# Kernel optimization log

Hardware: AMD Instinct MI355X
Metric: run time of the kernel (lower is better)

The kernel has to match this reference:

```python
import jax, jax.numpy as jnp
import numpy as np

T = 2048        # tokens
HID = 4096      # hidden_size
H = 32          # num attention heads
KV = 8          # num key/value heads (GQA)
D = HID // H    # head_dim = 128
THETA = 10000.0


def setup_inputs() -> dict:
    key = jax.random.key(0)
    k1, k2, k3 = jax.random.split(key, 3)
    hidden_states = jax.random.normal(k1, (T, HID), jnp.float32)
    positions = jnp.arange(T, dtype=jnp.int32)
    Wqkv = jax.random.normal(k2, ((H + 2 * KV) * D, HID), jnp.float32) * 0.02
    Wo = jax.random.normal(k3, (HID, H * D), jnp.float32) * 0.02
    return {"hidden_states": hidden_states, "positions": positions,
            "Wqkv": Wqkv, "Wo": Wo}


def _rope(positions, x):
    """Neox-style rotary embedding. x: [T, h, D], positions: [T]."""
    half = D // 2
    inv_freq = 1.0 / (THETA ** (jnp.arange(half, dtype=jnp.float32) / half))
    ang = positions.astype(jnp.float32)[:, None] * inv_freq      # [T, half]
    cos = jnp.cos(ang)[:, None, :]                                # [T, 1, half]
    sin = jnp.sin(ang)[:, None, :]
    x1, x2 = x[..., :half], x[..., half:]
    return jnp.concatenate([x1 * cos - x2 * sin, x2 * cos + x1 * sin], axis=-1)


def reference(hidden_states, positions, Wqkv, Wo):
    # fused QKV projection (no bias)
    qkv = hidden_states @ Wqkv.T                                  # [T, (H+2KV)*D]
    q, k, v = jnp.split(qkv, [H * D, H * D + KV * D], axis=1)
    q = q.reshape(T, H, D)
    k = k.reshape(T, KV, D)
    v = v.reshape(T, KV, D)
    # RoPE on q and k
    q = _rope(positions, q)
    k = _rope(positions, k)
    # GQA: expand kv heads to match q heads
    g = H // KV
    k = jnp.repeat(k, g, axis=1)                                  # [T, H, D]
    v = jnp.repeat(v, g, axis=1)
    # causal attention (flash-attention math)
    scores = jnp.einsum('thd,shd->hts', q, k) * (D ** -0.5)       # [H, T, T]
    causal = jnp.tril(jnp.ones((T, T), dtype=bool))
    scores = jnp.where(causal[None], scores, jnp.float32(-1e30))
    probs = jax.nn.softmax(scores, axis=-1)
    attn = jnp.einsum('hts,shd->thd', probs, v).reshape(T, H * D)
    # output projection
    return attn @ Wo.T
```

## Files before the change

kernel.cpp:

```cpp
#include <hip/hip_runtime.h>
#include <stdint.h>

#define T_SEQ 2048
#define HIDDEN 4096
#define NHEAD 32
#define NKV 8
#define HDIM 128
#define QKVN 6144

typedef __bf16 bf16x8 __attribute__((ext_vector_type(8)));
typedef float f32x4 __attribute__((ext_vector_type(4)));
typedef unsigned short u16;
typedef u16 u16x8 __attribute__((ext_vector_type(8)));
typedef u16 u16x4 __attribute__((ext_vector_type(4)));

__device__ __forceinline__ u16 f2bf(float f) {
  uint32_t u = __builtin_bit_cast(uint32_t, f);
  u = (u + 0x7fffu + ((u >> 16) & 1u)) >> 16;
  return (u16)u;
}
__device__ __forceinline__ float bf2f(u16 h) {
  uint32_t u = ((uint32_t)h) << 16;
  return __builtin_bit_cast(float, u);
}

__device__ __forceinline__ void gload16(const void* g, void* l) {
  __builtin_amdgcn_global_load_lds(
      (__attribute__((address_space(1))) void*)(uintptr_t)g,
      (__attribute__((address_space(3))) void*)(uintptr_t)l, 16, 0, 0);
}

__global__ void cvt2_kernel(const float* __restrict__ in1, u16* __restrict__ out1, int n1_4,
                            const float* __restrict__ in2, u16* __restrict__ out2, int n2_4) {
  int base = blockIdx.x * blockDim.x + threadIdx.x;
  int stride = gridDim.x * blockDim.x;
  for (int i = base; i < n1_4; i += stride) {
    float4 v = ((const float4*)in1)[i];
    u16x4 o;
    o.x = f2bf(v.x); o.y = f2bf(v.y); o.z = f2bf(v.z); o.w = f2bf(v.w);
    ((u16x4*)out1)[i] = o;
  }
  for (int i = base; i < n2_4; i += stride) {
    float4 v = ((const float4*)in2)[i];
    u16x4 o;
    o.x = f2bf(v.x); o.y = f2bf(v.y); o.z = f2bf(v.z); o.w = f2bf(v.w);
    ((u16x4*)out2)[i] = o;
  }
}

__global__ void prep_kernel(u16* __restrict__ qkv, const int* __restrict__ pos,
                            u16* __restrict__ vt,
                            const float* __restrict__ wo_in, u16* __restrict__ wo_out,
                            int wo_n4) {
  __shared__ u16 tile[64][64];
  const int bid = blockIdx.x;
  const int tid = threadIdx.x;

  if (bid < 512) {
    const int tb = bid & 31;
    const int yy = bid >> 5;
    const int kvh = yy >> 1;
    const int d0 = (yy & 1) * 64;
    const u16* src = qkv + (size_t)(NHEAD + NKV) * HDIM + kvh * HDIM + d0;
#pragma unroll
    for (int g = 0; g < 2; ++g) {
      int u = g * 256 + tid;
      int t = u >> 3, ds = u & 7;
      u16x8 v = *(const u16x8*)(src + (size_t)(tb * 64 + t) * QKVN + ds * 8);
#pragma unroll
      for (int j = 0; j < 8; ++j) {
        int d = ds * 8 + j;
        tile[d][(((t >> 3) ^ (d & 7)) * 8) + (t & 7)] = v[j];
      }
    }
    __syncthreads();
    u16* dst = vt + ((size_t)kvh * HDIM + d0) * T_SEQ + tb * 64;
#pragma unroll
    for (int g = 0; g < 4; ++g) {
      int u = g * 256 + tid;
      int d = u >> 4, qd = u & 15;
      int a = qd >> 3, gg = (qd >> 1) & 3, b = qd & 1;
      int t0 = 32 * a + 16 * b + 4 * gg;
      u16x4 v = *(const u16x4*)&tile[d][(((t0 >> 3) ^ (d & 7)) * 8) + (t0 & 7)];
      *(u16x4*)(dst + (size_t)d * T_SEQ + qd * 4) = v;
    }
    return;
  }

  const int nb = gridDim.x - 512;
  const int base = (bid - 512) * blockDim.x + tid;
  const int stride = nb * blockDim.x;
  for (int idx = base; idx < T_SEQ * 40 * 64; idx += stride) {
    int i = idx & 63;
    int head = (idx >> 6) % 40;
    int t = idx / (40 * 64);
    int hb = head < NHEAD ? head * HDIM : NHEAD * HDIM + (head - NHEAD) * HDIM;
    float p = (float)pos[t];
    float inv_freq = exp2f(-(float)i * (13.287712379549449f / 64.0f));
    float ang = p * inv_freq;
    float s, c;
    sincosf(ang, &s, &c);
    u16* p1 = qkv + (size_t)t * QKVN + hb + i;
    u16* p2 = p1 + 64;
    float x1 = bf2f(*p1), x2 = bf2f(*p2);
    *p1 = f2bf(x1 * c - x2 * s);
    *p2 = f2bf(x2 * c + x1 * s);
  }
  for (int i = base; i < wo_n4; i += stride) {
    float4 v = ((const float4*)wo_in)[i];
    u16x4 o;
    o.x = f2bf(v.x); o.y = f2bf(v.y); o.z = f2bf(v.z); o.w = f2bf(v.w);
    ((u16x4*)wo_out)[i] = o;
  }
}

__device__ __forceinline__ void storeC(float* p, float v) { *p = v; }
__device__ __forceinline__ void storeC(u16* p, float v) { *p = f2bf(v); }
__device__ __forceinline__ f32x4 mfma16(bf16x8 a, bf16x8 b, f32x4 c) {
  return __builtin_amdgcn_mfma_f32_16x16x32_bf16(a, b, c, 0, 0, 0);
}

__global__ void __launch_bounds__(512, 1)
gemm_qkv(const u16* __restrict__ A, const u16* __restrict__ B,
         u16* __restrict__ C, int M, int N, int K) {
  __shared__ u16 As_[2][128 * 64];
  __shared__ u16 Bs_[2][384 * 64];

  const int tid = threadIdx.x;
  const int lane = tid & 63;
  const int w = tid >> 6;
  const int wr = w >> 2, wc = w & 3;
  const int l15 = lane & 15, lg = lane >> 4;

  const int c8 = blockIdx.x & 7, i8 = blockIdx.x >> 3;
  const int by = i8 & 15;
  const int bx = c8 * 2 + (i8 >> 4);
  const int bm = by * 128, bn = bx * 384;

  const int u_lo = w * 64 + lane, u_hi = u_lo + 512;
  const int r0 = u_lo >> 3, s0 = (u_lo & 7) ^ (r0 & 7);
  const int r1 = u_hi >> 3, s1 = (u_hi & 7) ^ (r1 & 7);
  const u16* a_s0 = A + (size_t)(bm + r0) * K + s0 * 8;
  const u16* a_s1 = A + (size_t)(bm + r1) * K + s1 * 8;
  const u16* b_s0[3];
  const u16* b_s1[3];
#pragma unroll
  for (int h = 0; h < 3; ++h) {
    b_s0[h] = B + (size_t)(bn + h * 128 + r0) * K + s0 * 8;
    b_s1[h] = B + (size_t)(bn + h * 128 + r1) * K + s1 * 8;
  }

  const int ax = l15 & 7;
  const int sl0 = (lg ^ ax) * 8;
  const int sl1 = ((4 + lg) ^ ax) * 8;
  const int a_row = (wr * 64 + l15) * 64;
  const int b_row = (wc * 96 + l15) * 64;

  f32x4 acc[4][6] = {};
  bf16x8 af[4][2], bfr[6][2];

#define BARRIER() asm volatile("s_barrier" ::: "memory")
#define WAITBAR(n_) asm volatile("s_waitcnt vmcnt(" #n_ ")\n\ts_barrier" ::: "memory")
#define STAGE_A(t_, p_)                                                        \
  {                                                                            \
    gload16(a_s0 + (size_t)(t_) * 64, &As_[p_][w * 512]);                      \
    gload16(a_s1 + (size_t)(t_) * 64, &As_[p_][4096 + w * 512]);               \
  }
#define STAGE_B(t_, p_, h_)                                                    \
  {                                                                            \
    gload16(b_s0[h_] + (size_t)(t_) * 64, &Bs_[p_][(h_) * 8192 + w * 512]);    \
    gload16(b_s1[h_] + (size_t)(t_) * 64,                                      \
            &Bs_[p_][(h_) * 8192 + 4096 + w * 512]);                           \
  }

  STAGE_A(0, 0);
  STAGE_B(0, 0, 0); STAGE_B(0, 0, 1); STAGE_B(0, 0, 2);
  STAGE_B(1, 1, 0); STAGE_B(1, 1, 1); STAGE_B(1, 1, 2);
  WAITBAR(6);

  const int NT = K >> 6;
  for (int v = 0; v < NT; ++v) {
    const int cur = v & 1, alt = cur ^ 1;
    const u16* Ac = &As_[cur][0];
    const u16* Bc = &Bs_[cur][0];
    const bool s1ok = (v + 1) < NT, s2ok = (v + 2) < NT;

    {
      if (s1ok) STAGE_A(v + 1, alt);
#pragma unroll
      for (int mi = 0; mi < 2; ++mi) {
        af[mi][0] = *(const bf16x8*)&Ac[a_row + mi * 1024 + sl0];
        af[mi][1] = *(const bf16x8*)&Ac[a_row + mi * 1024 + sl1];
      }
#pragma unroll
      for (int ni = 0; ni < 3; ++ni) {
        bfr[ni][0] = *(const bf16x8*)&Bc[b_row + ni * 1024 + sl0];
        bfr[ni][1] = *(const bf16x8*)&Bc[b_row + ni * 1024 + sl1];
      }
      BARRIER();
      __builtin_amdgcn_s_setprio(1);
#pragma unroll
      for (int mi = 0; mi < 2; ++mi)
#pragma unroll
        for (int ni = 0; ni < 3; ++ni) {
          acc[mi][ni] = mfma16(af[mi][0], bfr[ni][0], acc[mi][ni]);
          acc[mi][ni] = mfma16(af[mi][1], bfr[ni][1], acc[mi][ni]);
        }
      __builtin_amdgcn_s_setprio(0);
      BARRIER();
    }
    {
#pragma unroll
      for (int ni = 3; ni < 6; ++ni) {
        bfr[ni][0] = *(const bf16x8*)&Bc[b_row + ni * 1024 + sl0];
        bfr[ni][1] = *(const bf16x8*)&Bc[b_row + ni * 1024 + sl1];
      }
      BARRIER();
      __builtin_amdgcn_s_setprio(1);
#pragma unroll
      for (int mi = 0; mi < 2; ++mi)
#pragma unroll
        for (int ni = 3; ni < 6; ++ni) {
          acc[mi][ni] = mfma16(af[mi][0], bfr[ni][0], acc[mi][ni]);
          acc[mi][ni] = mfma16(af[mi][1], bfr[ni][1], acc[mi][ni]);
        }
      __builtin_amdgcn_s_setprio(0);
      BARRIER();
    }
    {
      if (s2ok) { STAGE_B(v + 2, cur, 0); STAGE_B(v + 2, cur, 1); STAGE_B(v + 2, cur, 2); }
#pragma unroll
      for (int mi = 2; mi < 4; ++mi) {
        af[mi][0] = *(const bf16x8*)&Ac[a_row + mi * 1024 + sl0];
        af[mi][1] = *(const bf16x8*)&Ac[a_row + mi * 1024 + sl1];
      }
      BARRIER();
      __builtin_amdgcn_s_setprio(1);
#pragma unroll
      for (int mi = 2; mi < 4; ++mi)
#pragma unroll
        for (int ni = 0; ni < 6; ++ni) {
          acc[mi][ni] = mfma16(af[mi][0], bfr[ni][0], acc[mi][ni]);
          acc[mi][ni] = mfma16(af[mi][1], bfr[ni][1], acc[mi][ni]);
        }
      __builtin_amdgcn_s_setprio(0);
      if (s2ok) { WAITBAR(6); } else if (s1ok) { WAITBAR(0); } else { BARRIER(); }
    }
  }

#pragma unroll
  for (int mi = 0; mi < 4; ++mi)
#pragma unroll
    for (int ni = 0; ni < 6; ++ni)
#pragma unroll
      for (int r = 0; r < 4; ++r) {
        int row = bm + wr * 64 + mi * 16 + lg * 4 + r;
        int col = bn + wc * 96 + ni * 16 + l15;
        storeC(&C[(size_t)row * N + col], acc[mi][ni][r]);
      }
#undef STAGE_A
#undef STAGE_B
#undef WAITBAR
#undef BARRIER
}

template <typename OutT>
__global__ void __launch_bounds__(512, 2)
gemm256(const u16* __restrict__ A, const u16* __restrict__ B,
        OutT* __restrict__ C0, OutT* __restrict__ C1,
        int N, int K, int NT, int sliceBlocks,
        int nbx, int rw, int rh) {
  __shared__ u16 As_[2][256 * 64];
  __shared__ u16 Bs_[2][256 * 64];

  const int tid = threadIdx.x;
  const int lane = tid & 63;
  const int w = tid >> 6;
  const int wr = w >> 2, wc = w & 3;
  const int l15 = lane & 15, lg = lane >> 4;

  const int bid = blockIdx.x;
  const int slice = bid / sliceBlocks;
  const int wi = bid % sliceBlocks;
  const int k0 = slice * (NT << 6);
  OutT* __restrict__ C = slice ? C1 : C0;

  const int c8 = wi & 7, i8 = wi >> 3;
  const int rpr = nbx / rw;
  const int by = (c8 / rpr) * rh + (i8 % rh);
  const int bx = (c8 % rpr) * rw + (i8 / rh);
  const int bm = by * 256, bn = bx * 256;

  const int u_lo = w * 64 + lane, u_hi = u_lo + 512;
  const int r0 = u_lo >> 3, s0 = (u_lo & 7) ^ (r0 & 7);
  const int r1 = u_hi >> 3, s1 = (u_hi & 7) ^ (r1 & 7);
  const u16* a0s0 = A + (size_t)(bm + r0) * K + k0 + s0 * 8;
  const u16* a0s1 = A + (size_t)(bm + r1) * K + k0 + s1 * 8;
  const u16* a1s0 = A + (size_t)(bm + 128 + r0) * K + k0 + s0 * 8;
  const u16* a1s1 = A + (size_t)(bm + 128 + r1) * K + k0 + s1 * 8;
  const u16* b0s0 = B + (size_t)(bn + r0) * K + k0 + s0 * 8;
  const u16* b0s1 = B + (size_t)(bn + r1) * K + k0 + s1 * 8;
  const u16* b1s0 = B + (size_t)(bn + 128 + r0) * K + k0 + s0 * 8;
  const u16* b1s1 = B + (size_t)(bn + 128 + r1) * K + k0 + s1 * 8;

  const int ax = l15 & 7;
  const int sl0 = (lg ^ ax) * 8;
  const int sl1 = ((4 + lg) ^ ax) * 8;
  const int a_row = (wr * 128 + l15) * 64;
  const int b_row = (wc * 64 + l15) * 64;

  f32x4 acc[8][4] = {};
  bf16x8 bfr[4][2];

#define BARRIER() asm volatile("s_barrier" ::: "memory")
#define WAITBAR(n_) asm volatile("s_waitcnt vmcnt(" #n_ ")\n\ts_barrier" ::: "memory")
#define STAGE_HALF(p0_, p1_, dst_, t_)                                         \
  {                                                                            \
    gload16((p0_) + (size_t)(t_) * 64, (dst_) + (size_t)w * 512);              \
    gload16((p1_) + (size_t)(t_) * 64, (dst_) + 4096 + (size_t)w * 512);       \
  }

  STAGE_HALF(a0s0, a0s1, &As_[0][0], 0);
  STAGE_HALF(a1s0, a1s1, &As_[0][8192], 0);
  STAGE_HALF(b0s0, b0s1, &Bs_[0][0], 0);
  STAGE_HALF(b1s0, b1s1, &Bs_[0][8192], 0);
  STAGE_HALF(b0s0, b0s1, &Bs_[1][0], 1);
  STAGE_HALF(b1s0, b1s1, &Bs_[1][8192], 1);
  WAITBAR(4);

  for (int v = 0; v < NT; ++v) {
    const int cur = v & 1, alt = cur ^ 1;
    const u16* Ac = &As_[cur][0];
    const u16* Bc = &Bs_[cur][0];
    const bool s1ok = (v + 1) < NT, s2ok = (v + 2) < NT;

#define MFMA_QUAD(p_, A0_, A1_, A2_, A3_)                                      \
    __builtin_amdgcn_s_setprio(1);                                             \
    _Pragma("unroll") for (int ni = 0; ni < 4; ++ni) {                         \
      acc[2 * (p_)][ni] = mfma16(A0_, bfr[ni][0], acc[2 * (p_)][ni]);          \
      acc[2 * (p_)][ni] = mfma16(A1_, bfr[ni][1], acc[2 * (p_)][ni]);          \
      acc[2 * (p_) + 1][ni] = mfma16(A2_, bfr[ni][0], acc[2 * (p_) + 1][ni]);  \
      acc[2 * (p_) + 1][ni] = mfma16(A3_, bfr[ni][1], acc[2 * (p_) + 1][ni]);  \
    }                                                                          \
    __builtin_amdgcn_s_setprio(0);

    {
#pragma unroll
      for (int ni = 0; ni < 4; ++ni) {
        bfr[ni][0] = *(const bf16x8*)&Bc[b_row + ni * 1024 + sl0];
        bfr[ni][1] = *(const bf16x8*)&Bc[b_row + ni * 1024 + sl1];
      }
      bf16x8 f0 = *(const bf16x8*)&Ac[a_row + 0 * 1024 + sl0];
      bf16x8 f1 = *(const bf16x8*)&Ac[a_row + 0 * 1024 + sl1];
      bf16x8 f2 = *(const bf16x8*)&Ac[a_row + 1 * 1024 + sl0];
      bf16x8 f3 = *(const bf16x8*)&Ac[a_row + 1 * 1024 + sl1];
      if (s1ok) STAGE_HALF(a0s0, a0s1, &As_[alt][0], v + 1);
      BARRIER();
      MFMA_QUAD(0, f0, f1, f2, f3);
      BARRIER();
    }
    {
      bf16x8 f0 = *(const bf16x8*)&Ac[a_row + 2 * 1024 + sl0];
      bf16x8 f1 = *(const bf16x8*)&Ac[a_row + 2 * 1024 + sl1];
      bf16x8 f2 = *(const bf16x8*)&Ac[a_row + 3 * 1024 + sl0];
      bf16x8 f3 = *(const bf16x8*)&Ac[a_row + 3 * 1024 + sl1];
      if (s1ok) STAGE_HALF(a1s0, a1s1, &As_[alt][8192], v + 1);
      if (s2ok) STAGE_HALF(b0s0, b0s1, &Bs_[cur][0], v + 2);
      BARRIER();
      MFMA_QUAD(1, f0, f1, f2, f3);
      BARRIER();
    }
    {
      bf16x8 f0 = *(const bf16x8*)&Ac[a_row + 4 * 1024 + sl0];
      bf16x8 f1 = *(const bf16x8*)&Ac[a_row + 4 * 1024 + sl1];
      bf16x8 f2 = *(const bf16x8*)&Ac[a_row + 5 * 1024 + sl0];
      bf16x8 f3 = *(const bf16x8*)&Ac[a_row + 5 * 1024 + sl1];
      if (s2ok) STAGE_HALF(b1s0, b1s1, &Bs_[cur][8192], v + 2);
      BARRIER();
      MFMA_QUAD(2, f0, f1, f2, f3);
      BARRIER();
    }
    {
      bf16x8 f0 = *(const bf16x8*)&Ac[a_row + 6 * 1024 + sl0];
      bf16x8 f1 = *(const bf16x8*)&Ac[a_row + 6 * 1024 + sl1];
      bf16x8 f2 = *(const bf16x8*)&Ac[a_row + 7 * 1024 + sl0];
      bf16x8 f3 = *(const bf16x8*)&Ac[a_row + 7 * 1024 + sl1];
      BARRIER();
      MFMA_QUAD(3, f0, f1, f2, f3);
      if (s2ok) { WAITBAR(4); } else { WAITBAR(0); }
    }
#undef MFMA_QUAD
  }

#pragma unroll
  for (int mi = 0; mi < 8; ++mi)
#pragma unroll
    for (int ni = 0; ni < 4; ++ni)
#pragma unroll
      for (int r = 0; r < 4; ++r) {
        int row = bm + wr * 128 + mi * 16 + lg * 4 + r;
        int col = bn + wc * 64 + ni * 16 + l15;
        storeC(&C[(size_t)row * N + col], acc[mi][ni][r]);
      }
#undef STAGE_HALF
#undef WAITBAR
#undef BARRIER
}

__global__ void reduce_add(float* __restrict__ out, const float* __restrict__ part, int n4) {
  int i = blockIdx.x * blockDim.x + threadIdx.x;
  int stride = gridDim.x * blockDim.x;
  for (; i < n4; i += stride) {
    float4 a = ((const float4*)out)[i];
    float4 b = ((const float4*)part)[i];
    a.x += b.x; a.y += b.y; a.z += b.z; a.w += b.w;
    ((float4*)out)[i] = a;
  }
}

__global__ void __launch_bounds__(256, 2)
attn_kernel(const u16* __restrict__ qkv, const u16* __restrict__ vt,
            u16* __restrict__ out) {
  __shared__ u16 Ksh[2][64 * 128];
  __shared__ u16 Vsh[2][128 * 64];

  const int tid = threadIdx.x;
  const int lane = tid & 63;
  const int w = tid >> 6;
  const int l15 = lane & 15, lg = lane >> 4;

  const int bid = blockIdx.x;
  const int u8 = bid & 255, sfl = bid >> 8;
  const int kvh = u8 & 7;
  const int hg = (u8 >> 3) & 3;
  const int x = (u8 >> 5) & 7;
  const int qi = sfl ? x : (15 - x);
  const int h = kvh * 4 + hg;
  const int q0 = qi * 128;
  const int nt = 2 * qi + 2;
  const int wrow = q0 + w * 32;

  const u16* Kg = qkv + NHEAD * HDIM + kvh * HDIM;
  const u16* Vg = vt + (size_t)kvh * HDIM * T_SEQ;

  bf16x8 qa[2][4];
#pragma unroll
  for (int mi = 0; mi < 2; ++mi) {
    const u16* qrow = qkv + (size_t)(wrow + mi * 16 + l15) * QKVN + h * HDIM + lg * 8;
#pragma unroll
    for (int ks = 0; ks < 4; ++ks) qa[mi][ks] = *(const bf16x8*)(qrow + ks * 32);
  }

  f32x4 acc_o[2][8] = {};
  float m[2] = {-1e30f, -1e30f}, lsum[2] = {0.f, 0.f};

  const float scale = 0.088388347648318447f;

#define STAGE_K(kv0, p)                                                        \
  {                                                                            \
    _Pragma("unroll") for (int rnd = 0; rnd < 4; ++rnd) {                      \
      int cc = rnd * 256 + tid;                                                \
      int krow = cc >> 4, kslot = cc & 15;                                     \
      gload16(Kg + (size_t)((kv0) + krow) * QKVN + (kslot ^ (krow & 7)) * 8,   \
              &Ksh[p][(rnd * 256 + w * 64) * 8]);                              \
    }                                                                          \
  }
#define STAGE_V(kv0, p)                                                        \
  {                                                                            \
    _Pragma("unroll") for (int rnd = 0; rnd < 4; ++rnd) {                      \
      int cc = rnd * 256 + tid;                                                \
      int vrow = cc >> 3, ps = cc & 7;                                         \
      gload16(Vg + (size_t)vrow * T_SEQ + (kv0) + ((ps ^ (vrow & 7)) * 8),     \
              &Vsh[p][(rnd * 256 + w * 64) * 8]);                              \
    }                                                                          \
  }

  STAGE_K(0, 0);
  STAGE_V(0, 0);
  __syncthreads();

  for (int t = 0; t < nt; ++t) {
    const int p = t & 1;
    const int kv0 = t * 64;
    const bool more = (t + 1 < nt);
    if (more) {
      STAGE_K(kv0 + 64, p ^ 1);
      STAGE_V(kv0 + 64, p ^ 1);
    }

    if (kv0 <= wrow + 31) {
      f32x4 s[2][4] = {};
#pragma unroll
      for (int ks = 0; ks < 4; ++ks) {
#pragma unroll
        for (int n = 0; n < 4; ++n) {
          int row16 = n * 16 + l15;
          bf16x8 kf = *(const bf16x8*)&Ksh[p][row16 * 128 +
                                              (((ks * 4 + lg) ^ (row16 & 7)) * 8)];
          s[0][n] = mfma16(kf, qa[0][ks], s[0][n]);
          s[1][n] = mfma16(kf, qa[1][ks], s[1][n]);
        }
      }

      const bool diag = (kv0 + 63 > wrow);
      float mx[2];
#pragma unroll
      for (int mi = 0; mi < 2; ++mi) {
        float mm = -1e30f;
        int tq = wrow + mi * 16 + l15;
#pragma unroll
        for (int n = 0; n < 4; ++n)
#pragma unroll
          for (int r = 0; r < 4; ++r) {
            float v = s[mi][n][r] * scale;
            if (diag && (kv0 + n * 16 + lg * 4 + r) > tq) v = -1e30f;
            s[mi][n][r] = v;
            mm = fmaxf(mm, v);
          }
        mm = fmaxf(mm, __shfl_xor(mm, 16, 64));
        mm = fmaxf(mm, __shfl_xor(mm, 32, 64));
        mx[mi] = mm;
      }

      float alpha[2];
#pragma unroll
      for (int mi = 0; mi < 2; ++mi) {
        float mn = fmaxf(m[mi], mx[mi]);
        alpha[mi] = __expf(m[mi] - mn);
        m[mi] = mn;
        lsum[mi] *= alpha[mi];
      }
#pragma unroll
      for (int mi = 0; mi < 2; ++mi)
#pragma unroll
        for (int r = 0; r < 4; ++r) {
          float al = __shfl(alpha[mi], lg * 4 + r, 64);
#pragma unroll
          for (int nd = 0; nd < 8; ++nd) acc_o[mi][nd][r] *= al;
        }

      bf16x8 paf[2][2];
#pragma unroll
      for (int mi = 0; mi < 2; ++mi) {
        float ps = 0.f;
#pragma unroll
        for (int n = 0; n < 4; ++n)
#pragma unroll
          for (int r = 0; r < 4; ++r) {
            float pv = __expf(s[mi][n][r] - m[mi]);
            s[mi][n][r] = pv;
            ps += pv;
          }
        ps += __shfl_xor(ps, 16, 64);
        ps += __shfl_xor(ps, 32, 64);
        lsum[mi] += ps;
#pragma unroll
        for (int ks = 0; ks < 2; ++ks) {
          u16x8 pk;
#pragma unroll
          for (int hn = 0; hn < 2; ++hn)
#pragma unroll
            for (int r = 0; r < 4; ++r)
              pk[hn * 4 + r] = f2bf(s[mi][2 * ks + hn][r]);
          paf[mi][ks] = __builtin_bit_cast(bf16x8, pk);
        }
      }

#pragma unroll
      for (int ks = 0; ks < 2; ++ks) {
#pragma unroll
        for (int nd = 0; nd < 8; ++nd) {
          int d = nd * 16 + l15;
          bf16x8 bv = *(const bf16x8*)&Vsh[p][d * 64 + (((ks * 4 + lg) ^ (d & 7)) * 8)];
          acc_o[0][nd] = mfma16(paf[0][ks], bv, acc_o[0][nd]);
          acc_o[1][nd] = mfma16(paf[1][ks], bv, acc_o[1][nd]);
        }
      }
    }

    __syncthreads();
  }

#pragma unroll
  for (int mi = 0; mi < 2; ++mi)
#pragma unroll
    for (int r = 0; r < 4; ++r) {
      float ls = __shfl(lsum[mi], lg * 4 + r, 64);
      float inv = 1.f / ls;
      int row = wrow + mi * 16 + lg * 4 + r;
#pragma unroll
      for (int nd = 0; nd < 8; ++nd) {
        int col = h * HDIM + nd * 16 + l15;
        out[(size_t)row * (NHEAD * HDIM) + col] = f2bf(acc_o[mi][nd][r] * inv);
      }
    }
#undef STAGE_K
#undef STAGE_V
}

extern "C" void kernel_launch(void* const* d_in, const int* in_sizes, int n_in,
                              void* d_out, int out_size, void* d_ws, size_t ws_size,
                              hipStream_t stream) {
  const float* hs   = (const float*)d_in[0];
  const int*   pos  = (const int*)d_in[1];
  const float* wqkv = (const float*)d_in[2];
  const float* wo   = (const float*)d_in[3];
  float* out = (float*)d_out;
  uint8_t* ws = (uint8_t*)d_ws;

  if (ws_size < 142606336u) return;
  u16* hs_bf   = (u16*)(ws + 0);
  u16* wqkv_bf = (u16*)(ws + 16777216u);
  u16* wo_bf   = (u16*)(ws + 67108864u);
  u16* qkv_bf  = (u16*)(ws + 100663296u);
  u16* attn_bf = (u16*)(ws + 125829120u);
  float* part  = (float*)(ws + 16777216u);
  u16* vt_buf  = (u16*)(ws + 0);

  cvt2_kernel<<<2048, 256, 0, stream>>>(hs, hs_bf, (T_SEQ * HIDDEN) / 4,
                                        wqkv, wqkv_bf, (QKVN * HIDDEN) / 4);

  gemm_qkv<<<256, 512, 0, stream>>>(hs_bf, wqkv_bf, qkv_bf, T_SEQ, QKVN, HIDDEN);

  prep_kernel<<<2048, 256, 0, stream>>>(qkv_bf, pos, vt_buf,
                                        wo, wo_bf, (HIDDEN * HIDDEN) / 4);

  attn_kernel<<<512, 256, 0, stream>>>(qkv_bf, vt_buf, attn_bf);

  gemm256<float><<<256, 512, 0, stream>>>(
      attn_bf, wo_bf, out, part, HIDDEN, HIDDEN, 32, 128, 16, 2, 8);

  reduce_add<<<2048, 256, 0, stream>>>(out, part, (T_SEQ * HIDDEN) / 4);
}
```

Before: 318.4 us.

## Halve QKV GEMM k-tile, widen conversion and reduce kernels to 8 elements

The QKV GEMM now stages 32-wide k-slices instead of 64, which halves LDS use and lets the launch bounds allow more blocks per CU. The LDS swizzle and fragment loads are reworked to match, and the three compute phases per iteration collapse into two. The fp32-to-bf16 conversion and the split-K reduce kernels each process two float4 per thread per iteration. The smaller k-tile means twice as many barriers and loop iterations per unit of work, and the grid of 256 blocks may be too small to gain from the higher occupancy.

```diff
diff --git a/kernel.cpp b/kernel.cpp
--- a/kernel.cpp
+++ b/kernel.cpp
@@ -30,21 +30,25 @@
       (__attribute__((address_space(3))) void*)(uintptr_t)l, 16, 0, 0);
 }
 
-__global__ void cvt2_kernel(const float* __restrict__ in1, u16* __restrict__ out1, int n1_4,
-                            const float* __restrict__ in2, u16* __restrict__ out2, int n2_4) {
+__global__ void cvt2_kernel(const float* __restrict__ in1, u16* __restrict__ out1, int n1_8,
+                            const float* __restrict__ in2, u16* __restrict__ out2, int n2_8) {
   int base = blockIdx.x * blockDim.x + threadIdx.x;
   int stride = gridDim.x * blockDim.x;
-  for (int i = base; i < n1_4; i += stride) {
-    float4 v = ((const float4*)in1)[i];
-    u16x4 o;
-    o.x = f2bf(v.x); o.y = f2bf(v.y); o.z = f2bf(v.z); o.w = f2bf(v.w);
-    ((u16x4*)out1)[i] = o;
-  }
-  for (int i = base; i < n2_4; i += stride) {
-    float4 v = ((const float4*)in2)[i];
-    u16x4 o;
-    o.x = f2bf(v.x); o.y = f2bf(v.y); o.z = f2bf(v.z); o.w = f2bf(v.w);
-    ((u16x4*)out2)[i] = o;
+  for (int i = base; i < n1_8; i += stride) {
+    float4 a = ((const float4*)in1)[2 * i];
+    float4 b = ((const float4*)in1)[2 * i + 1];
+    u16x8 o;
+    o[0] = f2bf(a.x); o[1] = f2bf(a.y); o[2] = f2bf(a.z); o[3] = f2bf(a.w);
+    o[4] = f2bf(b.x); o[5] = f2bf(b.y); o[6] = f2bf(b.z); o[7] = f2bf(b.w);
+    ((u16x8*)out1)[i] = o;
+  }
+  for (int i = base; i < n2_8; i += stride) {
+    float4 a = ((const float4*)in2)[2 * i];
+    float4 b = ((const float4*)in2)[2 * i + 1];
+    u16x8 o;
+    o[0] = f2bf(a.x); o[1] = f2bf(a.y); o[2] = f2bf(a.z); o[3] = f2bf(a.w);
+    o[4] = f2bf(b.x); o[5] = f2bf(b.y); o[6] = f2bf(b.z); o[7] = f2bf(b.w);
+    ((u16x8*)out2)[i] = o;
   }
 }
 
@@ -120,11 +124,11 @@
   return __builtin_amdgcn_mfma_f32_16x16x32_bf16(a, b, c, 0, 0, 0);
 }
 
-__global__ void __launch_bounds__(512, 1)
+__global__ void __launch_bounds__(512, 4)
 gemm_qkv(const u16* __restrict__ A, const u16* __restrict__ B,
          u16* __restrict__ C, int M, int N, int K) {
-  __shared__ u16 As_[2][128 * 64];
-  __shared__ u16 Bs_[2][384 * 64];
+  __shared__ u16 As_[2][128 * 32];
+  __shared__ u16 Bs_[2][384 * 32];
 
   const int tid = threadIdx.x;
   const int lane = tid & 63;
@@ -137,48 +141,42 @@
   const int bx = c8 * 2 + (i8 >> 4);
   const int bm = by * 128, bn = bx * 384;
 
-  const int u_lo = w * 64 + lane, u_hi = u_lo + 512;
-  const int r0 = u_lo >> 3, s0 = (u_lo & 7) ^ (r0 & 7);
-  const int r1 = u_hi >> 3, s1 = (u_hi & 7) ^ (r1 & 7);
-  const u16* a_s0 = A + (size_t)(bm + r0) * K + s0 * 8;
-  const u16* a_s1 = A + (size_t)(bm + r1) * K + s1 * 8;
-  const u16* b_s0[3];
-  const u16* b_s1[3];
-#pragma unroll
-  for (int h = 0; h < 3; ++h) {
-    b_s0[h] = B + (size_t)(bn + h * 128 + r0) * K + s0 * 8;
-    b_s1[h] = B + (size_t)(bn + h * 128 + r1) * K + s1 * 8;
-  }
-
-  const int ax = l15 & 7;
-  const int sl0 = (lg ^ ax) * 8;
-  const int sl1 = ((4 + lg) ^ ax) * 8;
-  const int a_row = (wr * 64 + l15) * 64;
-  const int b_row = (wc * 96 + l15) * 64;
+  const int ua = w * 64 + lane;
+  const int ra = ua >> 2;
+  const int sa = (ua & 3) ^ (ra & 3) ^ ((ra >> 2) & 3);
+  const u16* a_src = A + (size_t)(bm + ra) * K + sa * 8;
+  const u16* b_src[3];
+#pragma unroll
+  for (int g = 0; g < 3; ++g) {
+    int u = g * 512 + w * 64 + lane;
+    int r = u >> 2;
+    int s = (u & 3) ^ (r & 3) ^ ((r >> 2) & 3);
+    b_src[g] = B + (size_t)(bn + r) * K + s * 8;
+  }
+
+  const int sl = (lg ^ (l15 & 3) ^ ((l15 >> 2) & 3)) * 8;
+  const int a_rd = (wr * 64 + l15) * 32 + sl;
+  const int b_rd = (wc * 96 + l15) * 32 + sl;
 
   f32x4 acc[4][6] = {};
-  bf16x8 af[4][2], bfr[6][2];
+  bf16x8 af[4], bfr[6];
 
 #define BARRIER() asm volatile("s_barrier" ::: "memory")
 #define WAITBAR(n_) asm volatile("s_waitcnt vmcnt(" #n_ ")\n\ts_barrier" ::: "memory")
-#define STAGE_A(t_, p_)                                                        \
+#define STAGE_A(t_, p_) gload16(a_src + (size_t)(t_) * 32, &As_[p_][w * 512]);
+#define STAGE_B(t_, p_)                                                        \
   {                                                                            \
-    gload16(a_s0 + (size_t)(t_) * 64, &As_[p_][w * 512]);                      \
-    gload16(a_s1 + (size_t)(t_) * 64, &As_[p_][4096 + w * 512]);               \
-  }
-#define STAGE_B(t_, p_, h_)                                                    \
-  {                                                                            \
-    gload16(b_s0[h_] + (size_t)(t_) * 64, &Bs_[p_][(h_) * 8192 + w * 512]);    \
-    gload16(b_s1[h_] + (size_t)(t_) * 64,                                      \
-            &Bs_[p_][(h_) * 8192 + 4096 + w * 512]);                           \
+    gload16(b_src[0] + (size_t)(t_) * 32, &Bs_[p_][w * 512]);                  \
+    gload16(b_src[1] + (size_t)(t_) * 32, &Bs_[p_][4096 + w * 512]);           \
+    gload16(b_src[2] + (size_t)(t_) * 32, &Bs_[p_][8192 + w * 512]);           \
   }
 
   STAGE_A(0, 0);
-  STAGE_B(0, 0, 0); STAGE_B(0, 0, 1); STAGE_B(0, 0, 2);
-  STAGE_B(1, 1, 0); STAGE_B(1, 1, 1); STAGE_B(1, 1, 2);
-  WAITBAR(6);
-
-  const int NT = K >> 6;
+  STAGE_B(0, 0);
+  STAGE_B(1, 1);
+  WAITBAR(3);
+
+  const int NT = K >> 5;
   for (int v = 0; v < NT; ++v) {
     const int cur = v & 1, alt = cur ^ 1;
     const u16* Ac = &As_[cur][0];
@@ -188,63 +186,32 @@
     {
       if (s1ok) STAGE_A(v + 1, alt);
 #pragma unroll
-      for (int mi = 0; mi < 2; ++mi) {
-        af[mi][0] = *(const bf16x8*)&Ac[a_row + mi * 1024 + sl0];
-        af[mi][1] = *(const bf16x8*)&Ac[a_row + mi * 1024 + sl1];
-      }
-#pragma unroll
-      for (int ni = 0; ni < 3; ++ni) {
-        bfr[ni][0] = *(const bf16x8*)&Bc[b_row + ni * 1024 + sl0];
-        bfr[ni][1] = *(const bf16x8*)&Bc[b_row + ni * 1024 + sl1];
-      }
+      for (int mi = 0; mi < 4; ++mi) af[mi] = *(const bf16x8*)&Ac[a_rd + mi * 512];
+#pragma unroll
+      for (int ni = 0; ni < 3; ++ni) bfr[ni] = *(const bf16x8*)&Bc[b_rd + ni * 512];
       BARRIER();
       __builtin_amdgcn_s_setprio(1);
 #pragma unroll
-      for (int mi = 0; mi < 2; ++mi)
-#pragma unroll
-        for (int ni = 0; ni < 3; ++ni) {
-          acc[mi][ni] = mfma16(af[mi][0], bfr[ni][0], acc[mi][ni]);
-          acc[mi][ni] = mfma16(af[mi][1], bfr[ni][1], acc[mi][ni]);
-        }
+      for (int mi = 0; mi < 4; ++mi)
+#pragma unroll
+        for (int ni = 0; ni < 3; ++ni)
+          acc[mi][ni] = mfma16(af[mi], bfr[ni], acc[mi][ni]);
       __builtin_amdgcn_s_setprio(0);
       BARRIER();
     }
     {
 #pragma unroll
-      for (int ni = 3; ni < 6; ++ni) {
-        bfr[ni][0] = *(const bf16x8*)&Bc[b_row + ni * 1024 + sl0];
-        bfr[ni][1] = *(const bf16x8*)&Bc[b_row + ni * 1024 + sl1];
-      }
-      BARRIER();
+      for (int ni = 3; ni < 6; ++ni) bfr[ni] = *(const bf16x8*)&Bc[b_rd + ni * 512];
+      BARRIER();
+      if (s2ok) STAGE_B(v + 2, cur);
       __builtin_amdgcn_s_setprio(1);
 #pragma unroll
-      for (int mi = 0; mi < 2; ++mi)
-#pragma unroll
-        for (int ni = 3; ni < 6; ++ni) {
-          acc[mi][ni] = mfma16(af[mi][0], bfr[ni][0], acc[mi][ni]);
-          acc[mi][ni] = mfma16(af[mi][1], bfr[ni][1], acc[mi][ni]);
-        }
+      for (int mi = 0; mi < 4; ++mi)
+#pragma unroll
+        for (int ni = 3; ni < 6; ++ni)
+          acc[mi][ni] = mfma16(af[mi], bfr[ni], acc[mi][ni]);
       __builtin_amdgcn_s_setprio(0);
-      BARRIER();
-    }
-    {
-      if (s2ok) { STAGE_B(v + 2, cur, 0); STAGE_B(v + 2, cur, 1); STAGE_B(v + 2, cur, 2); }
-#pragma unroll
-      for (int mi = 2; mi < 4; ++mi) {
-        af[mi][0] = *(const bf16x8*)&Ac[a_row + mi * 1024 + sl0];
-        af[mi][1] = *(const bf16x8*)&Ac[a_row + mi * 1024 + sl1];
-      }
-      BARRIER();
-      __builtin_amdgcn_s_setprio(1);
-#pragma unroll
-      for (int mi = 2; mi < 4; ++mi)
-#pragma unroll
-        for (int ni = 0; ni < 6; ++ni) {
-          acc[mi][ni] = mfma16(af[mi][0], bfr[ni][0], acc[mi][ni]);
-          acc[mi][ni] = mfma16(af[mi][1], bfr[ni][1], acc[mi][ni]);
-        }
-      __builtin_amdgcn_s_setprio(0);
-      if (s2ok) { WAITBAR(6); } else if (s1ok) { WAITBAR(0); } else { BARRIER(); }
+      if (s2ok) { WAITBAR(3); } else if (s1ok) { WAITBAR(0); } else { BARRIER(); }
     }
   }
 
@@ -408,13 +375,17 @@
 }
 
 __global__ void reduce_add(float* __restrict__ out, const float* __restrict__ part, int n4) {
-  int i = blockIdx.x * blockDim.x + threadIdx.x;
-  int stride = gridDim.x * blockDim.x;
+  int i = (blockIdx.x * blockDim.x + threadIdx.x) * 2;
+  int stride = gridDim.x * blockDim.x * 2;
   for (; i < n4; i += stride) {
-    float4 a = ((const float4*)out)[i];
-    float4 b = ((const float4*)part)[i];
-    a.x += b.x; a.y += b.y; a.z += b.z; a.w += b.w;
-    ((float4*)out)[i] = a;
+    float4 a0 = ((const float4*)out)[i];
+    float4 b0 = ((const float4*)part)[i];
+    float4 a1 = ((const float4*)out)[i + 1];
+    float4 b1 = ((const float4*)part)[i + 1];
+    a0.x += b0.x; a0.y += b0.y; a0.z += b0.z; a0.w += b0.w;
+    a1.x += b1.x; a1.y += b1.y; a1.z += b1.z; a1.w += b1.w;
+    ((float4*)out)[i] = a0;
+    ((float4*)out)[i + 1] = a1;
   }
 }
 
@@ -617,8 +588,8 @@
   float* part  = (float*)(ws + 16777216u);
   u16* vt_buf  = (u16*)(ws + 0);
 
-  cvt2_kernel<<<2048, 256, 0, stream>>>(hs, hs_bf, (T_SEQ * HIDDEN) / 4,
-                                        wqkv, wqkv_bf, (QKVN * HIDDEN) / 4);
+  cvt2_kernel<<<2048, 256, 0, stream>>>(hs, hs_bf, (T_SEQ * HIDDEN) / 8,
+                                        wqkv, wqkv_bf, (QKVN * HIDDEN) / 8);
 
   gemm_qkv<<<256, 512, 0, stream>>>(hs_bf, wqkv_bf, qkv_bf, T_SEQ, QKVN, HIDDEN);
 
```

Measured after the change: 540.0 us. +69.6%, slower.
